# Kernel tuning notes

Measured on AMD Instinct MI355X. Metric: run time of the kernel, lower is better.

## Reference

```python
import jax, jax.numpy as jnp
import numpy as np


def setup_inputs() -> dict:
    key = jax.random.key(0)
    ks = jax.random.split(key, 6)
    B, HW, CIN, COUT, K = 256, 64, 3, 128, 32
    inputs = jax.random.normal(ks[0], (B, HW, HW, CIN), jnp.float32)
    conv_w = jax.random.normal(ks[1], (3, 3, CIN, COUT), jnp.float32) * 0.1
    conv_b = jnp.zeros((COUT,), jnp.float32)
    match_w = jax.random.normal(ks[2], (COUT,), jnp.float32) * 0.1
    match_b = jnp.zeros((1,), jnp.float32)
    pat_w = jax.random.normal(ks[3], (32 * 32 * K, 1), jnp.float32) * 0.01
    pat_b = jnp.zeros((1,), jnp.float32)
    base_w = jax.random.normal(ks[4], (32 * 32 * COUT, 3), jnp.float32) * 0.01
    base_b = jnp.zeros((3,), jnp.float32)
    pattern_set_index = jax.random.randint(ks[5], (K,), 0, COUT, jnp.int32)
    return {
        "inputs": inputs, "conv_w": conv_w, "conv_b": conv_b,
        "match_w": match_w, "match_b": match_b,
        "pat_w": pat_w, "pat_b": pat_b,
        "base_w": base_w, "base_b": base_b,
        "pattern_set_index": pattern_set_index,
    }


def reference(inputs, conv_w, conv_b, match_w, match_b,
              pat_w, pat_b, base_w, base_b, pattern_set_index):
    B = inputs.shape[0]
    # feat_extract: conv3x3 stride 2 + relu -> feats0 [B,32,32,128]; GAP -> feats1 [B,128]
    feats0 = jax.nn.relu(
        jax.lax.conv_general_dilated(
            inputs, conv_w, window_strides=(2, 2), padding='SAME',
            dimension_numbers=('NHWC', 'HWIO', 'NHWC')) + conv_b)
    feats1 = feats0.mean(axis=(1, 2))  # [B,128]
    # pat_matcher: boolean per-sample match mask
    matches = (feats1 @ match_w + match_b[0]) > 0.0  # [B] bool
    # pat_pred on channel-subset features (tf.gather axis=3)
    sel = jnp.take(feats0, pattern_set_index, axis=3)  # [B,32,32,32]
    p = jax.nn.sigmoid(sel.reshape(B, -1) @ pat_w + pat_b)[:, 0]  # [B]
    # BinaryToCategorical(pattern_class=0, num_classes=3): [p, (1-p)/2, (1-p)/2]
    o = (1.0 - p) * 0.5
    cat = jnp.stack([p, o, o], axis=-1)  # [B,3]
    # base_pred on full features (used for matched-low and non-matched samples)
    base = jax.nn.softmax(feats0.reshape(B, -1) @ base_w + base_b, axis=-1)  # [B,3]
    # route: matched AND pat score >= 0.5 -> categorized pat pred, else base pred
    use_pat = matches & (p >= 0.5)
    return jnp.where(use_pat[:, None], cat, base)
```

## Files before the change

### kernel.cpp

```cpp
#include <hip/hip_runtime.h>
#include <math.h>

#define TPB 512

__global__ __launch_bounds__(256)
void prep_weights(const float* __restrict__ base_w,
                  const float* __restrict__ pat_w,
                  const int*   __restrict__ psi,
                  float4* __restrict__ wq2)
{
    int idx = blockIdx.x * 256 + threadIdx.x;
    int hw = idx >> 7, c = idx & 127;
    const float* bp = base_w + (size_t)idx * 3;
    float b0 = bp[0], b1 = bp[1], b2 = bp[2];
    float pc = 0.f;
    const float* pr = pat_w + hw * 32;
    #pragma unroll
    for (int k = 0; k < 32; ++k)
        pc += (psi[k] == c) ? pr[k] : 0.f;
    wq2[(size_t)((hw >> 2) * 128 + c) * 4 + (hw & 3)] = make_float4(b0, b1, b2, pc);
}

__global__ __launch_bounds__(TPB, 6)
void pattern_branch_kernel(const float* __restrict__ in,
                           const float* __restrict__ conv_w,
                           const float* __restrict__ conv_b,
                           const float* __restrict__ match_w,
                           const float4* __restrict__ wq2,
                           float* __restrict__ part)
{
    constexpr int ROWF4 = 50;
    __shared__ float4 xlds4[17 * ROWF4];
    __shared__ float  red[8][5];

    const int bx  = blockIdx.x;
    const int qh  = bx >> 8;
    const int b   = bx & 255;
    const int tid = threadIdx.x;

    for (int s = tid; s < 17 * ROWF4; s += TPB) xlds4[s] = make_float4(0.f, 0.f, 0.f, 0.f);
    __syncthreads();
    const float4* inp4 = (const float4*)(in + (size_t)b * 12288);
    for (int s = tid; s < 17 * 48; s += TPB) {
        int r  = s / 48;
        int qq = s - r * 48;
        int ih = 16 * qh + r;
        if (ih < 64) xlds4[r * ROWF4 + qq] = inp4[ih * 48 + qq];
    }
    __syncthreads();

    const int c  = tid & 127;
    const int sg = tid >> 7;
    float w[27];
    #pragma unroll
    for (int k = 0; k < 27; ++k) w[k] = conv_w[k * 128 + c];
    float bias = conv_b[c];
    float mw   = match_w[c];
    #pragma unroll
    for (int k = 0; k < 27; ++k) asm volatile("" : "+v"(w[k]));
    asm volatile("" : "+v"(bias), "+v"(mw));

    float sm = 0.f, s0 = 0.f, s1 = 0.f, s2 = 0.f, sp = 0.f;

    const float4* wqp = wq2 + (size_t)((8 * qh + 2 * sg) * 8) * 512 / 4 * 4;
    wqp = wq2 + (size_t)((8 * qh + 2 * sg) * 8 * 128 + c) * 4;

    for (int it = 0; it < 16; ++it) {
        const int oh_loc = 2 * sg + (it >> 3);
        const int q      = it & 7;

        float acc0 = bias, acc1 = bias, acc2 = bias, acc3 = bias;
        #pragma unroll
        for (int kh = 0; kh < 3; ++kh) {
            const float4* rp = &xlds4[(4 * sg + 2 * (it >> 3) + kh) * ROWF4 + 6 * q];
            const float* wk = &w[kh * 9];
            {
                float4 t0 = rp[0], t1 = rp[1], t2 = rp[2], t3 = rp[3];
                acc0 = fmaf(t0.x, wk[0], acc0); acc0 = fmaf(t0.y, wk[1], acc0);
                acc0 = fmaf(t0.z, wk[2], acc0); acc0 = fmaf(t0.w, wk[3], acc0);
                acc0 = fmaf(t1.x, wk[4], acc0); acc0 = fmaf(t1.y, wk[5], acc0);
                acc0 = fmaf(t1.z, wk[6], acc0); acc0 = fmaf(t1.w, wk[7], acc0);
                acc0 = fmaf(t2.x, wk[8], acc0);
                acc1 = fmaf(t1.z, wk[0], acc1); acc1 = fmaf(t1.w, wk[1], acc1);
                acc1 = fmaf(t2.x, wk[2], acc1); acc1 = fmaf(t2.y, wk[3], acc1);
                acc1 = fmaf(t2.z, wk[4], acc1); acc1 = fmaf(t2.w, wk[5], acc1);
                acc1 = fmaf(t3.x, wk[6], acc1); acc1 = fmaf(t3.y, wk[7], acc1);
                acc1 = fmaf(t3.z, wk[8], acc1);
            }
            {
                float4 t3 = rp[3], t4 = rp[4], t5 = rp[5], t6 = rp[6];
                acc2 = fmaf(t3.x, wk[0], acc2); acc2 = fmaf(t3.y, wk[1], acc2);
                acc2 = fmaf(t3.z, wk[2], acc2); acc2 = fmaf(t3.w, wk[3], acc2);
                acc2 = fmaf(t4.x, wk[4], acc2); acc2 = fmaf(t4.y, wk[5], acc2);
                acc2 = fmaf(t4.z, wk[6], acc2); acc2 = fmaf(t4.w, wk[7], acc2);
                acc2 = fmaf(t5.x, wk[8], acc2);
                acc3 = fmaf(t4.z, wk[0], acc3); acc3 = fmaf(t4.w, wk[1], acc3);
                acc3 = fmaf(t5.x, wk[2], acc3); acc3 = fmaf(t5.y, wk[3], acc3);
                acc3 = fmaf(t5.z, wk[4], acc3); acc3 = fmaf(t5.w, wk[5], acc3);
                acc3 = fmaf(t6.x, wk[6], acc3); acc3 = fmaf(t6.y, wk[7], acc3);
                acc3 = fmaf(t6.z, wk[8], acc3);
            }
        }
        float4 wv0 = wqp[0], wv1 = wqp[1], wv2 = wqp[2], wv3 = wqp[3];
        wqp += 512;

        float f0 = fmaxf(acc0, 0.f), f1 = fmaxf(acc1, 0.f);
        float f2 = fmaxf(acc2, 0.f), f3 = fmaxf(acc3, 0.f);
        sm = fmaf(mw, (f0 + f1) + (f2 + f3), sm);
        s0 = fmaf(f0, wv0.x, s0); s1 = fmaf(f0, wv0.y, s1);
        s2 = fmaf(f0, wv0.z, s2); sp = fmaf(f0, wv0.w, sp);
        s0 = fmaf(f1, wv1.x, s0); s1 = fmaf(f1, wv1.y, s1);
        s2 = fmaf(f1, wv1.z, s2); sp = fmaf(f1, wv1.w, sp);
        s0 = fmaf(f2, wv2.x, s0); s1 = fmaf(f2, wv2.y, s1);
        s2 = fmaf(f2, wv2.z, s2); sp = fmaf(f2, wv2.w, sp);
        s0 = fmaf(f3, wv3.x, s0); s1 = fmaf(f3, wv3.y, s1);
        s2 = fmaf(f3, wv3.z, s2); sp = fmaf(f3, wv3.w, sp);
        (void)oh_loc; (void)q;
    }

    float vals[5] = { sm, s0, s1, s2, sp };
    #pragma unroll
    for (int off = 32; off > 0; off >>= 1)
        #pragma unroll
        for (int v = 0; v < 5; ++v)
            vals[v] += __shfl_down(vals[v], off, 64);
    int wv = tid >> 6, lane = tid & 63;
    if (lane == 0) {
        #pragma unroll
        for (int v = 0; v < 5; ++v) red[wv][v] = vals[v];
    }
    __syncthreads();
    if (tid == 0) {
        #pragma unroll
        for (int v = 0; v < 5; ++v) {
            float t = 0.f;
            for (int wj = 0; wj < 8; ++wj) t += red[wj][v];
            part[(qh * 5 + v) * 256 + b] = t;
        }
    }
}

__global__ __launch_bounds__(256)
void finalize_kernel(const float* __restrict__ part,
                     const float* __restrict__ match_b,
                     const float* __restrict__ pat_b,
                     const float* __restrict__ base_b,
                     float* __restrict__ out)
{
    int b = threadIdx.x;
    float t[5] = { 0.f, 0.f, 0.f, 0.f, 0.f };
    #pragma unroll
    for (int j = 0; j < 4; ++j)
        #pragma unroll
        for (int v = 0; v < 5; ++v)
            t[v] += part[(j * 5 + v) * 256 + b];
    float score = t[0] * (1.f / 1024.f) + match_b[0];
    float p = 1.f / (1.f + expf(-(t[4] + pat_b[0])));
    float l0 = t[1] + base_b[0], l1 = t[2] + base_b[1], l2 = t[3] + base_b[2];
    float m = fmaxf(l0, fmaxf(l1, l2));
    float e0 = expf(l0 - m), e1 = expf(l1 - m), e2 = expf(l2 - m);
    float inv = 1.f / (e0 + e1 + e2);
    bool use_pat = (score > 0.f) && (p >= 0.5f);
    float o0, o1, o2;
    if (use_pat) { o0 = p; o1 = 0.5f * (1.f - p); o2 = o1; }
    else         { o0 = e0 * inv; o1 = e1 * inv; o2 = e2 * inv; }
    out[b * 3 + 0] = o0;
    out[b * 3 + 1] = o1;
    out[b * 3 + 2] = o2;
}

extern "C" void kernel_launch(void* const* d_in, const int* in_sizes, int n_in,
                              void* d_out, int out_size, void* d_ws, size_t ws_size,
                              hipStream_t stream) {
    const float* in      = (const float*)d_in[0];
    const float* conv_w  = (const float*)d_in[1];
    const float* conv_b  = (const float*)d_in[2];
    const float* match_w = (const float*)d_in[3];
    const float* match_b = (const float*)d_in[4];
    const float* pat_w   = (const float*)d_in[5];
    const float* pat_b   = (const float*)d_in[6];
    const float* base_w  = (const float*)d_in[7];
    const float* base_b  = (const float*)d_in[8];
    const int*   psi     = (const int*)d_in[9];
    float* out = (float*)d_out;

    float4* wq2  = (float4*)d_ws;
    float*  part = (float*)((char*)d_ws + (size_t)131072 * 16);

    prep_weights<<<512, 256, 0, stream>>>(base_w, pat_w, psi, wq2);

    int B = in_sizes[0] / (64 * 64 * 3);
    pattern_branch_kernel<<<4 * B, TPB, 0, stream>>>(
        in, conv_w, conv_b, match_w, wq2, part);

    finalize_kernel<<<1, 256, 0, stream>>>(part, match_b, pat_b, base_b, out);
}
```

Before: 123.5 us.

## Load conv input via scalar loads and process two samples per block

Replaces the LDS staging of input rows with inline-asm scalar (SMEM) loads that pull each input row segment straight into SGPRs, exploiting that the input window is uniform across the wavefront. Each block now handles two samples over 512 blocks, which halves how often the per-channel weight-head loads are issued and amortises conv weights across both samples. Partial sums are doubled to 10 per block and the finalize kernel's indexing is adapted. It drops the LDS barriers but relies on hand-written waitcnt asm and hard-coded offsets, and it lowers the occupancy hint from 6 to 4.

```diff
diff --git a/kernel.cpp b/kernel.cpp
--- a/kernel.cpp
+++ b/kernel.cpp
@@ -2,6 +2,85 @@
 #include <math.h>
 
 #define TPB 512
+
+typedef float vf16 __attribute__((ext_vector_type(16)));
+typedef float vf8  __attribute__((ext_vector_type(8)));
+typedef float vf4  __attribute__((ext_vector_type(4)));
+
+#define Z4 ((vf4){0.f, 0.f, 0.f, 0.f})
+
+#define ISSUE3(A, B, C, P, O16, O8, O4)                     \
+  asm volatile("s_load_dwordx16 %0, %3, " O16 "\n\t"        \
+               "s_load_dwordx8  %1, %3, " O8 "\n\t"         \
+               "s_load_dwordx4  %2, %3, " O4                \
+               : "=&s"(A), "=&s"(B), "=&s"(C) : "s"(P))
+#define ISSUE2F(A, B, P, O16, O8)                           \
+  asm volatile("s_load_dwordx16 %0, %2, " O16 "\n\t"        \
+               "s_load_dwordx8  %1, %2, " O8                \
+               : "=&s"(A), "=&s"(B) : "s"(P))
+
+#define BIND6(A0, B0, C0, A1, B1, C1)                       \
+  asm volatile("s_waitcnt lgkmcnt(0)"                       \
+               : "+s"(A0), "+s"(B0), "+s"(C0),              \
+                 "+s"(A1), "+s"(B1), "+s"(C1))
+#define BIND4(A0, B0, A1, B1)                               \
+  asm volatile("s_waitcnt lgkmcnt(0)"                       \
+               : "+s"(A0), "+s"(B0), "+s"(A1), "+s"(B1))
+
+#define ROWFMA(A, B, C, K, U0, U1, U2, U3)                  \
+  do {                                                      \
+    U0 = fmaf(A[0],  w[K + 0], U0);                         \
+    U0 = fmaf(A[1],  w[K + 1], U0);                         \
+    U0 = fmaf(A[2],  w[K + 2], U0);                         \
+    U0 = fmaf(A[3],  w[K + 3], U0);                         \
+    U0 = fmaf(A[4],  w[K + 4], U0);                         \
+    U0 = fmaf(A[5],  w[K + 5], U0);                         \
+    U0 = fmaf(A[6],  w[K + 6], U0);                         \
+    U0 = fmaf(A[7],  w[K + 7], U0);                         \
+    U0 = fmaf(A[8],  w[K + 8], U0);                         \
+    U1 = fmaf(A[6],  w[K + 0], U1);                         \
+    U1 = fmaf(A[7],  w[K + 1], U1);                         \
+    U1 = fmaf(A[8],  w[K + 2], U1);                         \
+    U1 = fmaf(A[9],  w[K + 3], U1);                         \
+    U1 = fmaf(A[10], w[K + 4], U1);                         \
+    U1 = fmaf(A[11], w[K + 5], U1);                         \
+    U1 = fmaf(A[12], w[K + 6], U1);                         \
+    U1 = fmaf(A[13], w[K + 7], U1);                         \
+    U1 = fmaf(A[14], w[K + 8], U1);                         \
+    U2 = fmaf(A[12], w[K + 0], U2);                         \
+    U2 = fmaf(A[13], w[K + 1], U2);                         \
+    U2 = fmaf(A[14], w[K + 2], U2);                         \
+    U2 = fmaf(A[15], w[K + 3], U2);                         \
+    U2 = fmaf(B[0],  w[K + 4], U2);                         \
+    U2 = fmaf(B[1],  w[K + 5], U2);                         \
+    U2 = fmaf(B[2],  w[K + 6], U2);                         \
+    U2 = fmaf(B[3],  w[K + 7], U2);                         \
+    U2 = fmaf(B[4],  w[K + 8], U2);                         \
+    U3 = fmaf(B[2],  w[K + 0], U3);                         \
+    U3 = fmaf(B[3],  w[K + 1], U3);                         \
+    U3 = fmaf(B[4],  w[K + 2], U3);                         \
+    U3 = fmaf(B[5],  w[K + 3], U3);                         \
+    U3 = fmaf(B[6],  w[K + 4], U3);                         \
+    U3 = fmaf(B[7],  w[K + 5], U3);                         \
+    U3 = fmaf(C[0],  w[K + 6], U3);                         \
+    U3 = fmaf(C[1],  w[K + 7], U3);                         \
+    U3 = fmaf(C[2],  w[K + 8], U3);                         \
+  } while (0)
+
+#define HEADOP(U0, U1, U2, U3, SM, S0, S1, S2, SP)          \
+  do {                                                      \
+    float f0 = fmaxf(U0, 0.f), f1 = fmaxf(U1, 0.f);         \
+    float f2 = fmaxf(U2, 0.f), f3 = fmaxf(U3, 0.f);         \
+    SM = fmaf(mw, (f0 + f1) + (f2 + f3), SM);               \
+    S0 = fmaf(f0, qq0.x, S0); S1 = fmaf(f0, qq0.y, S1);     \
+    S2 = fmaf(f0, qq0.z, S2); SP = fmaf(f0, qq0.w, SP);     \
+    S0 = fmaf(f1, qq1.x, S0); S1 = fmaf(f1, qq1.y, S1);     \
+    S2 = fmaf(f1, qq1.z, S2); SP = fmaf(f1, qq1.w, SP);     \
+    S0 = fmaf(f2, qq2.x, S0); S1 = fmaf(f2, qq2.y, S1);     \
+    S2 = fmaf(f2, qq2.z, S2); SP = fmaf(f2, qq2.w, SP);     \
+    S0 = fmaf(f3, qq3.x, S0); S1 = fmaf(f3, qq3.y, S1);     \
+    S2 = fmaf(f3, qq3.z, S2); SP = fmaf(f3, qq3.w, SP);     \
+  } while (0)
 
 __global__ __launch_bounds__(256)
 void prep_weights(const float* __restrict__ base_w,
@@ -21,7 +100,7 @@
     wq2[(size_t)((hw >> 2) * 128 + c) * 4 + (hw & 3)] = make_float4(b0, b1, b2, pc);
 }
 
-__global__ __launch_bounds__(TPB, 6)
+__global__ __launch_bounds__(TPB, 4)
 void pattern_branch_kernel(const float* __restrict__ in,
                            const float* __restrict__ conv_w,
                            const float* __restrict__ conv_b,
@@ -29,114 +108,109 @@
                            const float4* __restrict__ wq2,
                            float* __restrict__ part)
 {
-    constexpr int ROWF4 = 50;
-    __shared__ float4 xlds4[17 * ROWF4];
-    __shared__ float  red[8][5];
+    __shared__ float red[8][10];
 
     const int bx  = blockIdx.x;
-    const int qh  = bx >> 8;
-    const int b   = bx & 255;
+    const int qh  = bx >> 7;
+    const int spr = bx & 127;
     const int tid = threadIdx.x;
-
-    for (int s = tid; s < 17 * ROWF4; s += TPB) xlds4[s] = make_float4(0.f, 0.f, 0.f, 0.f);
-    __syncthreads();
-    const float4* inp4 = (const float4*)(in + (size_t)b * 12288);
-    for (int s = tid; s < 17 * 48; s += TPB) {
-        int r  = s / 48;
-        int qq = s - r * 48;
-        int ih = 16 * qh + r;
-        if (ih < 64) xlds4[r * ROWF4 + qq] = inp4[ih * 48 + qq];
-    }
-    __syncthreads();
-
-    const int c  = tid & 127;
-    const int sg = tid >> 7;
+    const int c   = tid & 127;
+    const int sg  = __builtin_amdgcn_readfirstlane(tid) >> 7;
+
     float w[27];
     #pragma unroll
     for (int k = 0; k < 27; ++k) w[k] = conv_w[k * 128 + c];
     float bias = conv_b[c];
     float mw   = match_w[c];
-    #pragma unroll
-    for (int k = 0; k < 27; ++k) asm volatile("" : "+v"(w[k]));
-    asm volatile("" : "+v"(bias), "+v"(mw));
-
-    float sm = 0.f, s0 = 0.f, s1 = 0.f, s2 = 0.f, sp = 0.f;
-
-    const float4* wqp = wq2 + (size_t)((8 * qh + 2 * sg) * 8) * 512 / 4 * 4;
-    wqp = wq2 + (size_t)((8 * qh + 2 * sg) * 8 * 128 + c) * 4;
-
-    for (int it = 0; it < 16; ++it) {
-        const int oh_loc = 2 * sg + (it >> 3);
-        const int q      = it & 7;
-
-        float acc0 = bias, acc1 = bias, acc2 = bias, acc3 = bias;
-        #pragma unroll
-        for (int kh = 0; kh < 3; ++kh) {
-            const float4* rp = &xlds4[(4 * sg + 2 * (it >> 3) + kh) * ROWF4 + 6 * q];
-            const float* wk = &w[kh * 9];
-            {
-                float4 t0 = rp[0], t1 = rp[1], t2 = rp[2], t3 = rp[3];
-                acc0 = fmaf(t0.x, wk[0], acc0); acc0 = fmaf(t0.y, wk[1], acc0);
-                acc0 = fmaf(t0.z, wk[2], acc0); acc0 = fmaf(t0.w, wk[3], acc0);
-                acc0 = fmaf(t1.x, wk[4], acc0); acc0 = fmaf(t1.y, wk[5], acc0);
-                acc0 = fmaf(t1.z, wk[6], acc0); acc0 = fmaf(t1.w, wk[7], acc0);
-                acc0 = fmaf(t2.x, wk[8], acc0);
-                acc1 = fmaf(t1.z, wk[0], acc1); acc1 = fmaf(t1.w, wk[1], acc1);
-                acc1 = fmaf(t2.x, wk[2], acc1); acc1 = fmaf(t2.y, wk[3], acc1);
-                acc1 = fmaf(t2.z, wk[4], acc1); acc1 = fmaf(t2.w, wk[5], acc1);
-                acc1 = fmaf(t3.x, wk[6], acc1); acc1 = fmaf(t3.y, wk[7], acc1);
-                acc1 = fmaf(t3.z, wk[8], acc1);
+
+    const float* s0base = in + (size_t)(2 * spr) * 12288;
+    const float4* wqp = wq2 + ((size_t)(64 * qh + 16 * sg) * 128 + c) * 4;
+
+    float sm0 = 0.f, sa0 = 0.f, sb0 = 0.f, sc0 = 0.f, sp0 = 0.f;
+    float sm1 = 0.f, sa1 = 0.f, sb1 = 0.f, sc1 = 0.f, sp1 = 0.f;
+
+    #pragma unroll 1
+    for (int m = 0; m < 16; ++m) {
+        #pragma unroll
+        for (int k = 0; k < 27; ++k) asm volatile("" : "+v"(w[k]));
+        asm volatile("" : "+v"(bias), "+v"(mw));
+
+        const int oh = 8 * qh + 2 * sg + (m >> 3);
+        const int q  = m & 7;
+        const float* r0 = s0base + 2 * oh * 192 + 24 * q;
+        const bool qt   = (q < 7);
+        const bool r2ok = (oh < 31);
+
+        float4 qq0 = wqp[0], qq1 = wqp[1], qq2 = wqp[2], qq3 = wqp[3];
+        wqp += 512;
+
+        float u0 = bias, u1 = bias, u2 = bias, u3 = bias;
+        float t0 = bias, t1 = bias, t2 = bias, t3 = bias;
+
+        vf16 A0, A1; vf8 B0, B1; vf4 C0, C1;
+
+        if (qt) {
+            ISSUE3(A0, B0, C0, r0, "0", "64", "96");
+            ISSUE3(A1, B1, C1, r0, "49152", "49216", "49248");
+            BIND6(A0, B0, C0, A1, B1, C1);
+        } else {
+            ISSUE2F(A0, B0, r0, "0", "64");
+            ISSUE2F(A1, B1, r0, "49152", "49216");
+            C0 = Z4; C1 = Z4;
+            BIND4(A0, B0, A1, B1);
+        }
+        ROWFMA(A0, B0, C0, 0, u0, u1, u2, u3);
+        ROWFMA(A1, B1, C1, 0, t0, t1, t2, t3);
+
+        if (qt) {
+            ISSUE3(A0, B0, C0, r0, "768", "832", "864");
+            ISSUE3(A1, B1, C1, r0, "49920", "49984", "50016");
+            BIND6(A0, B0, C0, A1, B1, C1);
+        } else {
+            ISSUE2F(A0, B0, r0, "768", "832");
+            ISSUE2F(A1, B1, r0, "49920", "49984");
+            C0 = Z4; C1 = Z4;
+            BIND4(A0, B0, A1, B1);
+        }
+        ROWFMA(A0, B0, C0, 9, u0, u1, u2, u3);
+        ROWFMA(A1, B1, C1, 9, t0, t1, t2, t3);
+
+        if (r2ok) {
+            if (qt) {
+                ISSUE3(A0, B0, C0, r0, "1536", "1600", "1632");
+                ISSUE3(A1, B1, C1, r0, "50688", "50752", "50784");
+                BIND6(A0, B0, C0, A1, B1, C1);
+            } else {
+                ISSUE2F(A0, B0, r0, "1536", "1600");
+                ISSUE2F(A1, B1, r0, "50688", "50752");
+                C0 = Z4; C1 = Z4;
+                BIND4(A0, B0, A1, B1);
             }
-            {
-                float4 t3 = rp[3], t4 = rp[4], t5 = rp[5], t6 = rp[6];
-                acc2 = fmaf(t3.x, wk[0], acc2); acc2 = fmaf(t3.y, wk[1], acc2);
-                acc2 = fmaf(t3.z, wk[2], acc2); acc2 = fmaf(t3.w, wk[3], acc2);
-                acc2 = fmaf(t4.x, wk[4], acc2); acc2 = fmaf(t4.y, wk[5], acc2);
-                acc2 = fmaf(t4.z, wk[6], acc2); acc2 = fmaf(t4.w, wk[7], acc2);
-                acc2 = fmaf(t5.x, wk[8], acc2);
-                acc3 = fmaf(t4.z, wk[0], acc3); acc3 = fmaf(t4.w, wk[1], acc3);
-                acc3 = fmaf(t5.x, wk[2], acc3); acc3 = fmaf(t5.y, wk[3], acc3);
-                acc3 = fmaf(t5.z, wk[4], acc3); acc3 = fmaf(t5.w, wk[5], acc3);
-                acc3 = fmaf(t6.x, wk[6], acc3); acc3 = fmaf(t6.y, wk[7], acc3);
-                acc3 = fmaf(t6.z, wk[8], acc3);
-            }
+            ROWFMA(A0, B0, C0, 18, u0, u1, u2, u3);
+            ROWFMA(A1, B1, C1, 18, t0, t1, t2, t3);
         }
-        float4 wv0 = wqp[0], wv1 = wqp[1], wv2 = wqp[2], wv3 = wqp[3];
-        wqp += 512;
-
-        float f0 = fmaxf(acc0, 0.f), f1 = fmaxf(acc1, 0.f);
-        float f2 = fmaxf(acc2, 0.f), f3 = fmaxf(acc3, 0.f);
-        sm = fmaf(mw, (f0 + f1) + (f2 + f3), sm);
-        s0 = fmaf(f0, wv0.x, s0); s1 = fmaf(f0, wv0.y, s1);
-        s2 = fmaf(f0, wv0.z, s2); sp = fmaf(f0, wv0.w, sp);
-        s0 = fmaf(f1, wv1.x, s0); s1 = fmaf(f1, wv1.y, s1);
-        s2 = fmaf(f1, wv1.z, s2); sp = fmaf(f1, wv1.w, sp);
-        s0 = fmaf(f2, wv2.x, s0); s1 = fmaf(f2, wv2.y, s1);
-        s2 = fmaf(f2, wv2.z, s2); sp = fmaf(f2, wv2.w, sp);
-        s0 = fmaf(f3, wv3.x, s0); s1 = fmaf(f3, wv3.y, s1);
-        s2 = fmaf(f3, wv3.z, s2); sp = fmaf(f3, wv3.w, sp);
-        (void)oh_loc; (void)q;
+
+        HEADOP(u0, u1, u2, u3, sm0, sa0, sb0, sc0, sp0);
+        HEADOP(t0, t1, t2, t3, sm1, sa1, sb1, sc1, sp1);
     }
 
-    float vals[5] = { sm, s0, s1, s2, sp };
+    float vals[10] = { sm0, sa0, sb0, sc0, sp0, sm1, sa1, sb1, sc1, sp1 };
     #pragma unroll
     for (int off = 32; off > 0; off >>= 1)
         #pragma unroll
-        for (int v = 0; v < 5; ++v)
+        for (int v = 0; v < 10; ++v)
             vals[v] += __shfl_down(vals[v], off, 64);
-    int wv = tid >> 6, lane = tid & 63;
-    if (lane == 0) {
-        #pragma unroll
-        for (int v = 0; v < 5; ++v) red[wv][v] = vals[v];
+    int wv = tid >> 6;
+    if ((tid & 63) == 0) {
+        #pragma unroll
+        for (int v = 0; v < 10; ++v) red[wv][v] = vals[v];
     }
     __syncthreads();
-    if (tid == 0) {
-        #pragma unroll
-        for (int v = 0; v < 5; ++v) {
-            float t = 0.f;
-            for (int wj = 0; wj < 8; ++wj) t += red[wj][v];
-            part[(qh * 5 + v) * 256 + b] = t;
-        }
+    if (tid < 10) {
+        float t = 0.f;
+        #pragma unroll
+        for (int wj = 0; wj < 8; ++wj) t += red[wj][tid];
+        part[(qh * 10 + tid) * 128 + spr] = t;
     }
 }
 
@@ -147,13 +221,14 @@
                      const float* __restrict__ base_b,
                      float* __restrict__ out)
 {
-    int b = threadIdx.x;
+    int b   = threadIdx.x;
+    int s01 = b & 1, spr = b >> 1;
     float t[5] = { 0.f, 0.f, 0.f, 0.f, 0.f };
     #pragma unroll
     for (int j = 0; j < 4; ++j)
         #pragma unroll
         for (int v = 0; v < 5; ++v)
-            t[v] += part[(j * 5 + v) * 256 + b];
+            t[v] += part[(j * 10 + s01 * 5 + v) * 128 + spr];
     float score = t[0] * (1.f / 1024.f) + match_b[0];
     float p = 1.f / (1.f + expf(-(t[4] + pat_b[0])));
     float l0 = t[1] + base_b[0], l1 = t[2] + base_b[1], l2 = t[3] + base_b[2];
@@ -189,8 +264,7 @@
 
     prep_weights<<<512, 256, 0, stream>>>(base_w, pat_w, psi, wq2);
 
-    int B = in_sizes[0] / (64 * 64 * 3);
-    pattern_branch_kernel<<<4 * B, TPB, 0, stream>>>(
+    pattern_branch_kernel<<<512, TPB, 0, stream>>>(
         in, conv_w, conv_b, match_w, wq2, part);
 
     finalize_kernel<<<1, 256, 0, stream>>>(part, match_b, pat_b, base_b, out);
```

Result: slower. 131.7 us (+6.6%).
